# Kernel tuning notes

Hardware: AMD Instinct MI355X
Metric: run time of the kernel (lower is better)

The kernel has to match this reference:

```python
import jax, jax.numpy as jnp
import numpy as np

WS = 11        # gaussian window size
SIGMA = 1.5    # gaussian sigma
L = 10.0       # val_range
SSIM_C1 = (0.01 * L) ** 2
SSIM_C2 = (0.03 * L) ** 2


def _window():
    g = jnp.exp(-((jnp.arange(WS) - WS // 2) ** 2) / (2.0 * SIGMA ** 2))
    g = g / g.sum()
    return jnp.outer(g, g).astype(jnp.float32)  # [11,11], sums to 1


def _blur(z, win):
    # depthwise 11x11 gaussian blur with VALID padding; z: [..., H, W]
    lead = z.shape[:-2]
    zf = z.reshape((-1, 1) + z.shape[-2:])
    out = jax.lax.conv_general_dilated(zf, win[None, None], (1, 1), 'VALID')
    return out.reshape(lead + out.shape[-2:])


def setup_inputs() -> dict:
    key = jax.random.key(0)
    ks = jax.random.split(key, 7)
    B, C, Fc, H, W = 8, 64, 3, 192, 192
    return {
        'x': jax.random.normal(ks[0], (B, C, H, W), jnp.float32),
        'x_feature': jax.random.normal(ks[1], (B, Fc, H, W), jnp.float32),
        'spatial_w': jax.random.normal(ks[2], (1, Fc, 3, 1), jnp.float32) * 0.1,
        'W1': jax.random.normal(ks[3], (C, C), jnp.float32) * 0.05,
        'b1': jnp.zeros((C,), jnp.float32),
        'W2': jax.random.normal(ks[4], (C, C), jnp.float32) * 0.05,
        'b2': jnp.zeros((C,), jnp.float32),
    }


def reference(x, x_feature, spatial_w, W1, b1, W2, b2):
    win = _window()
    # per-channel gaussian moments (computed once, reused across all pairs)
    mu_x = _blur(x, win)                         # [B,C,h,w]
    mu_f = _blur(x_feature, win)                 # [B,F,h,w]
    sig_x = _blur(x * x, win) - mu_x ** 2        # variance of x channels
    sig_f = _blur(x_feature * x_feature, win) - mu_f ** 2
    # all pairwise cross-covariances in one batched blur
    prod = x_feature[:, :, None] * x[:, None]    # [B,F,C,H,W]
    sig_fx = _blur(prod, win) - mu_f[:, :, None] * mu_x[:, None]
    v1 = 2.0 * sig_fx + SSIM_C2
    v2 = sig_f[:, :, None] + sig_x[:, None] + SSIM_C2
    num = (2.0 * mu_f[:, :, None] * mu_x[:, None] + SSIM_C1) * v1
    den = (mu_f[:, :, None] ** 2 + mu_x[:, None] ** 2 + SSIM_C1) * v2
    ssim_info = (num / den).mean(axis=(-2, -1))  # [B,F,C]
    # spatial gate: Conv2d(3,1,(3,1),padding=(1,0)) over [B,F,C,1]
    si4 = ssim_info[..., None]                   # [B,F,C,1]
    h = jax.lax.conv_general_dilated(si4, spatial_w, (1, 1), ((1, 1), (0, 0)))
    h = jax.nn.relu(h).reshape(x.shape[0], -1)   # [B,C]
    h = jax.nn.relu(h @ W1.T + b1) @ W2.T + b2
    return jax.nn.sigmoid(h), ssim_info
```

## Files before the change

### kernel.cpp

```cpp
#include <hip/hip_runtime.h>
#include <math.h>

#define HW 192
#define OW 182
#define NPIX (OW*OW)
#define NTILE 8
#define SSIM_C1 0.01f
#define SSIM_C2 0.09f

#define Gk0 0.0010283835f
#define Gk1 0.0075987615f
#define Gk2 0.0360007700f
#define Gk3 0.1093608000f
#define Gk4 0.2130055400f
#define Gk5 0.2660117000f

typedef float v2f __attribute__((ext_vector_type(2)));

__device__ __forceinline__ v2f vfma(float w, v2f a, v2f b) {
    return __builtin_elementwise_fma((v2f){w, w}, a, b);
}
__device__ __forceinline__ v2f vfma2(v2f w, v2f a, v2f b) {
    return __builtin_elementwise_fma(w, a, b);
}

__device__ __forceinline__ void dgauss(float g[11]) {
    float s = 0.f;
#pragma unroll
    for (int i = 0; i < 11; ++i) {
        float d = (float)(i - 5);
        g[i] = expf(-(d * d) / 4.5f);
        s += g[i];
    }
    float inv = 1.f / s;
#pragma unroll
    for (int i = 0; i < 11; ++i) g[i] *= inv;
}

__global__ __launch_bounds__(256) void muf_kernel(const float* __restrict__ xf,
                                                  float* __restrict__ muf,
                                                  float* __restrict__ sigc2f) {
    const int tile = blockIdx.x % 14;
    const int img  = blockIdx.x / 14;
    const int r0   = tile * 13;

    __shared__ float raw[23][192];
    __shared__ float hb[2][23][184];

    float g[11]; dgauss(g);
    const int t = threadIdx.x;
    const float* src = xf + (size_t)img * HW * HW;

    for (int i = t; i < 23 * 192; i += 256) {
        int rr = i / 192, col = i - rr * 192;
        raw[rr][col] = src[(r0 + rr) * HW + col];
    }
    __syncthreads();

    for (int i = t; i < 23 * OW; i += 256) {
        int rr = i / OW, co = i - rr * OW;
        float a0 = 0.f, a1 = 0.f;
#pragma unroll
        for (int k = 0; k < 11; ++k) {
            float v = raw[rr][co + k];
            float w = g[k];
            a0 += w * v;
            a1 += w * v * v;
        }
        hb[0][rr][co] = a0;
        hb[1][rr][co] = a1;
    }
    __syncthreads();

    for (int i = t; i < 13 * OW; i += 256) {
        int rr = i / OW, co = i - rr * OW;
        float m = 0.f, s2 = 0.f;
#pragma unroll
        for (int k = 0; k < 11; ++k) {
            float w = g[k];
            m  += w * hb[0][rr + k][co];
            s2 += w * hb[1][rr + k][co];
        }
        size_t o = (size_t)img * NPIX + (size_t)(r0 + rr) * OW + co;
        muf[o]    = m;
        sigc2f[o] = s2 - m * m + SSIM_C2;
    }
}

__global__ __launch_bounds__(192, 4) void ssim_kernel(const float* __restrict__ x,
                                                      const float* __restrict__ xf,
                                                      const float* __restrict__ muf,
                                                      const float* __restrict__ sigc2f,
                                                      float* __restrict__ part) {
    const float G[11] = {Gk0,Gk1,Gk2,Gk3,Gk4,Gk5,Gk4,Gk3,Gk2,Gk1,Gk0};
    const v2f WA[6] = {{G[0],0.f},{G[2],G[1]},{G[4],G[3]},{G[6],G[5]},{G[8],G[7]},{G[10],G[9]}};
    const v2f WB[6] = {{G[1],G[0]},{G[3],G[2]},{G[5],G[4]},{G[7],G[6]},{G[9],G[8]},{0.f,G[10]}};

    const int blk  = blockIdx.x;
    const int c    = blk & 63;
    const int tile = (blk >> 6) & 7;
    const int b    = blk >> 9;

    const int out0  = (tile * 182) >> 3;
    const int out1  = ((tile + 1) * 182) >> 3;
    const int n_out = out1 - out0;

    const int t    = threadIdx.x;
    const int half = (t >= 96) ? 1 : 0;
    const int u    = half ? (t - 96) : t;
    const int cu   = 2 * u;
    const bool act = (u <= 90);

    const float* xp  = x  + ((size_t)(b * 64 + c)) * HW * HW + (size_t)out0 * HW + t;
    const float* fp0 = xf + ((size_t)(b * 3 + 0)) * HW * HW + (size_t)out0 * HW + t;
    const float* fp1 = fp0 + HW * HW;
    const float* fp2 = fp1 + HW * HW;

    const float* mp = muf    + (size_t)(b * 3) * NPIX + (size_t)(out0 + half) * OW + cu;
    const float* cp = sigc2f + (size_t)(b * 3) * NPIX + (size_t)(out0 + half) * OW + cu;

    __shared__ float eb[4][5][192];
    __shared__ float red[3][3];

    v2f P01[10], P23[10];
    float P4[10];
#pragma unroll
    for (int j = 0; j < 10; ++j) { P01[j] = (v2f){0.f,0.f}; P23[j] = (v2f){0.f,0.f}; P4[j] = 0.f; }

    v2f A0 = {0.f,0.f}, A1 = {0.f,0.f}, A2 = {0.f,0.f};

    v2f eE01, eE23; float eE4;

    auto vstep = [&](float xv, float a0, float a1, float a2, bool emit) {
        v2f v01 = {xv, xv * xv};
        v2f v23 = {xv * a0, xv * a1};
        float v4 = xv * a2;
        if (emit) {
            eE01 = vfma(G[10], v01, P01[0]);
            eE23 = vfma(G[10], v23, P23[0]);
            eE4  = fmaf(G[10], v4, P4[0]);
        }
#pragma unroll
        for (int j = 0; j < 9; ++j) {
            P01[j] = vfma(G[9 - j], v01, P01[j + 1]);
            P23[j] = vfma(G[9 - j], v23, P23[j + 1]);
            P4[j]  = fmaf(G[9 - j], v4, P4[j + 1]);
        }
        P01[9] = G[0] * v01;
        P23[9] = G[0] * v23;
        P4[9]  = G[0] * v4;
    };

    auto ssim2 = [&](const v2f mux, const v2f sigc,
                     const v2f mf, const v2f cc, const v2f h, v2f& A) {
        const v2f mux2 = mux * mux;
        v2f t1  = mf * mux;
        v2f sfx = h - t1;
        v2f v1s = vfma(2.f, sfx, (v2f){SSIM_C2, SSIM_C2});
        v2f n1  = vfma(2.f, t1, (v2f){SSIM_C1, SSIM_C1});
        v2f num = n1 * v1s;
        v2f qd  = vfma2(mf, mf, (v2f){SSIM_C1, SSIM_C1});
        v2f den = (qd + mux2) * (cc + sigc);
        v2f inv = {__builtin_amdgcn_rcpf(den.x), __builtin_amdgcn_rcpf(den.y)};
        A = vfma2(num, inv, A);
    };

#pragma unroll 1
    for (int r = 0; r < 10; r += 2) {
        float xA = xp[0],  aA0 = fp0[0],  aA1 = fp1[0],  aA2 = fp2[0];
        float xB = xp[HW], aB0 = fp0[HW], aB1 = fp1[HW], aB2 = fp2[HW];
        xp += 2 * HW; fp0 += 2 * HW; fp1 += 2 * HW; fp2 += 2 * HW;
        vstep(xA, aA0, aA1, aA2, false);
        vstep(xB, aB0, aB1, aB2, false);
    }

    const int n_pair = n_out >> 1;

    float xA = xp[0],  aA0 = fp0[0],  aA1 = fp1[0],  aA2 = fp2[0];
    float xB = xp[HW], aB0 = fp0[HW], aB1 = fp1[HW], aB2 = fp2[HW];

#pragma unroll 1
    for (int p = 0; p < n_pair; ++p) {
        const int rb = 2 * (p + 1);
        const int r1 = (rb     < n_out) ? rb     : (n_out - 1);
        const int r2 = (rb + 1 < n_out) ? rb + 1 : (n_out - 1);
        const int o1 = r1 * HW, o2 = r2 * HW;
        const float nxA = xp[o1], naA0 = fp0[o1], naA1 = fp1[o1], naA2 = fp2[o1];
        const float nxB = xp[o2], naB0 = fp0[o2], naB1 = fp1[o2], naB2 = fp2[o2];

        v2f mf0, mf1, mf2, cc0, cc1, cc2;
        if (act) {
            mf0 = *(const v2f*)(mp);
            mf1 = *(const v2f*)(mp + NPIX);
            mf2 = *(const v2f*)(mp + 2 * NPIX);
            cc0 = *(const v2f*)(cp);
            cc1 = *(const v2f*)(cp + NPIX);
            cc2 = *(const v2f*)(cp + 2 * NPIX);
            mp += 2 * OW; cp += 2 * OW;
        }

        const int e = 2 * p;
        const int sA = e & 3, sB = (e + 1) & 3;
        vstep(xA, aA0, aA1, aA2, true);
        eb[sA][0][t] = eE01.x; eb[sA][1][t] = eE01.y;
        eb[sA][2][t] = eE23.x; eb[sA][3][t] = eE23.y;
        eb[sA][4][t] = eE4;
        vstep(xB, aB0, aB1, aB2, true);
        eb[sB][0][t] = eE01.x; eb[sB][1][t] = eE01.y;
        eb[sB][2][t] = eE23.x; eb[sB][3][t] = eE23.y;
        eb[sB][4][t] = eE4;
        __syncthreads();

        xA = nxA; aA0 = naA0; aA1 = naA1; aA2 = naA2;
        xB = nxB; aB0 = naB0; aB1 = naB1; aB2 = naB2;

        if (act) {
            const int sH = half ? sB : sA;
            v2f hacc[5];
#pragma unroll
            for (int f = 0; f < 5; ++f) {
                const float* ep = &eb[sH][f][cu];
                v2f a = {0.f, 0.f};
#pragma unroll
                for (int m = 0; m < 6; ++m) {
                    v2f rd = *(const v2f*)(ep + 2 * m);
                    a = vfma2(WA[m], __builtin_shufflevector(rd, rd, 0, 0), a);
                    a = vfma2(WB[m], __builtin_shufflevector(rd, rd, 1, 1), a);
                }
                hacc[f] = a;
            }
            const v2f mux  = hacc[0];
            const v2f sigc = hacc[1] - mux * mux;
            ssim2(mux, sigc, mf0, cc0, hacc[2], A0);
            ssim2(mux, sigc, mf1, cc1, hacc[3], A1);
            ssim2(mux, sigc, mf2, cc2, hacc[4], A2);
        }
    }

    if (n_out & 1) {
        const int e = n_out - 1;
        vstep(xA, aA0, aA1, aA2, true);
        const int sA = e & 3;
        eb[sA][0][t] = eE01.x; eb[sA][1][t] = eE01.y;
        eb[sA][2][t] = eE23.x; eb[sA][3][t] = eE23.y;
        eb[sA][4][t] = eE4;
        __syncthreads();
        if (act && half == 0) {
            v2f mf0 = *(const v2f*)(mp);
            v2f mf1 = *(const v2f*)(mp + NPIX);
            v2f mf2 = *(const v2f*)(mp + 2 * NPIX);
            v2f cc0 = *(const v2f*)(cp);
            v2f cc1 = *(const v2f*)(cp + NPIX);
            v2f cc2 = *(const v2f*)(cp + 2 * NPIX);
            v2f hacc[5];
#pragma unroll
            for (int f = 0; f < 5; ++f) {
                const float* ep = &eb[sA][f][cu];
                v2f a = {0.f, 0.f};
#pragma unroll
                for (int m = 0; m < 6; ++m) {
                    v2f rd = *(const v2f*)(ep + 2 * m);
                    a = vfma2(WA[m], __builtin_shufflevector(rd, rd, 0, 0), a);
                    a = vfma2(WB[m], __builtin_shufflevector(rd, rd, 1, 1), a);
                }
                hacc[f] = a;
            }
            const v2f mux  = hacc[0];
            const v2f sigc = hacc[1] - mux * mux;
            ssim2(mux, sigc, mf0, cc0, hacc[2], A0);
            ssim2(mux, sigc, mf1, cc1, hacc[3], A1);
            ssim2(mux, sigc, mf2, cc2, hacc[4], A2);
        }
    }

    float acc0 = A0.x + A0.y;
    float acc1 = A1.x + A1.y;
    float acc2 = A2.x + A2.y;
#pragma unroll
    for (int off = 32; off > 0; off >>= 1) {
        acc0 += __shfl_down(acc0, off);
        acc1 += __shfl_down(acc1, off);
        acc2 += __shfl_down(acc2, off);
    }
    const int wid = t >> 6, lane = t & 63;
    if (lane == 0) { red[0][wid] = acc0; red[1][wid] = acc1; red[2][wid] = acc2; }
    __syncthreads();
    if (t == 0) {
        const size_t o = (size_t)tile * 1536 + (size_t)b * 192;
        part[o +   0 + c] = red[0][0] + red[0][1] + red[0][2];
        part[o +  64 + c] = red[1][0] + red[1][1] + red[1][2];
        part[o + 128 + c] = red[2][0] + red[2][1] + red[2][2];
    }
}

__global__ __launch_bounds__(64) void gate_kernel(const float* __restrict__ part,
                                                  const float* __restrict__ sw,
                                                  const float* __restrict__ W1,
                                                  const float* __restrict__ b1,
                                                  const float* __restrict__ W2,
                                                  const float* __restrict__ b2,
                                                  float* __restrict__ out,
                                                  float* __restrict__ out_ssim) {
    const int b = blockIdx.x;
    const int c = threadIdx.x;

    __shared__ float s[3][64];
    __shared__ float h0[64];
    __shared__ float h1[64];

    const float inv = 1.f / (float)NPIX;
#pragma unroll
    for (int f = 0; f < 3; ++f) {
        const int i = b * 192 + f * 64 + c;
        float v = 0.f;
#pragma unroll
        for (int k = 0; k < NTILE; ++k) v += part[i + k * 1536];
        v *= inv;
        s[f][c] = v;
        out_ssim[i] = v;
    }
    __syncthreads();

    float a = 0.f;
#pragma unroll
    for (int f = 0; f < 3; ++f)
#pragma unroll
        for (int i = 0; i < 3; ++i) {
            int cc = c - 1 + i;
            if (cc >= 0 && cc < 64) a += sw[f * 3 + i] * s[f][cc];
        }
    h0[c] = fmaxf(a, 0.f);
    __syncthreads();

    float a1 = b1[c];
    for (int j = 0; j < 64; ++j) a1 += W1[c * 64 + j] * h0[j];
    h1[c] = fmaxf(a1, 0.f);
    __syncthreads();

    float a2 = b2[c];
    for (int j = 0; j < 64; ++j) a2 += W2[c * 64 + j] * h1[j];
    out[b * 64 + c] = 1.f / (1.f + expf(-a2));
}

extern "C" void kernel_launch(void* const* d_in, const int* in_sizes, int n_in,
                              void* d_out, int out_size, void* d_ws, size_t ws_size,
                              hipStream_t stream) {
    const float* x  = (const float*)d_in[0];
    const float* xf = (const float*)d_in[1];
    const float* sw = (const float*)d_in[2];
    const float* W1 = (const float*)d_in[3];
    const float* b1 = (const float*)d_in[4];
    const float* W2 = (const float*)d_in[5];
    const float* b2 = (const float*)d_in[6];
    float* out = (float*)d_out;

    float* muf  = (float*)d_ws;
    float* sigf = muf + 24 * NPIX;
    float* part = sigf + 24 * NPIX;

    muf_kernel <<<24 * 14,        256, 0, stream>>>(xf, muf, sigf);
    ssim_kernel<<<8 * 64 * NTILE, 192, 0, stream>>>(x, xf, muf, sigf, part);
    gate_kernel<<<8,               64, 0, stream>>>(part, sw, W1, b1, W2, b2, out, out + 512);
}
```

Before: 108.5 us.

## Software-pipeline vertical blur with horizontal pass across shared-memory slots

Restructures the main loop so the vertical blur and shared-memory store for the next row pair overlap with the horizontal blur and SSIM math on the current pair. A prologue fills slots 0/1 first, and each iteration needs one barrier instead of a barrier between producing and consuming. Part of the LDS reads are issued before the vstep work to hide their latency. This raises register pressure (30 v2f LDS values held in flight) and adds more intricate slot and row-index bookkeeping.

```diff
diff --git a/kernel.cpp b/kernel.cpp
--- a/kernel.cpp
+++ b/kernel.cpp
@@ -104,6 +104,7 @@
     const int out0  = (tile * 182) >> 3;
     const int out1  = ((tile + 1) * 182) >> 3;
     const int n_out = out1 - out0;
+    const int n_in  = n_out + 10;
 
     const int t    = threadIdx.x;
     const int half = (t >= 96) ? 1 : 0;
@@ -151,9 +152,18 @@
         P4[9]  = G[0] * v4;
     };
 
-    auto ssim2 = [&](const v2f mux, const v2f sigc,
+    auto hblur = [&](const v2f rd[6]) {
+        v2f a = {0.f, 0.f};
+#pragma unroll
+        for (int m = 0; m < 6; ++m) {
+            a = vfma2(WA[m], __builtin_shufflevector(rd[m], rd[m], 0, 0), a);
+            a = vfma2(WB[m], __builtin_shufflevector(rd[m], rd[m], 1, 1), a);
+        }
+        return a;
+    };
+
+    auto ssim2 = [&](const v2f mux, const v2f mux2, const v2f sigc,
                      const v2f mf, const v2f cc, const v2f h, v2f& A) {
-        const v2f mux2 = mux * mux;
         v2f t1  = mf * mux;
         v2f sfx = h - t1;
         v2f v1s = vfma(2.f, sfx, (v2f){SSIM_C2, SSIM_C2});
@@ -165,6 +175,12 @@
         A = vfma2(num, inv, A);
     };
 
+    auto store_e = [&](int slot) {
+        eb[slot][0][t] = eE01.x; eb[slot][1][t] = eE01.y;
+        eb[slot][2][t] = eE23.x; eb[slot][3][t] = eE23.y;
+        eb[slot][4][t] = eE4;
+    };
+
 #pragma unroll 1
     for (int r = 0; r < 10; r += 2) {
         float xA = xp[0],  aA0 = fp0[0],  aA1 = fp1[0],  aA2 = fp2[0];
@@ -176,17 +192,26 @@
 
     const int n_pair = n_out >> 1;
 
-    float xA = xp[0],  aA0 = fp0[0],  aA1 = fp1[0],  aA2 = fp2[0];
-    float xB = xp[HW], aB0 = fp0[HW], aB1 = fp1[HW], aB2 = fp2[HW];
+    {
+        float xA = xp[0],  aA0 = fp0[0],  aA1 = fp1[0],  aA2 = fp2[0];
+        float xB = xp[HW], aB0 = fp0[HW], aB1 = fp1[HW], aB2 = fp2[HW];
+        xp += 2 * HW; fp0 += 2 * HW; fp1 += 2 * HW; fp2 += 2 * HW;
+        vstep(xA, aA0, aA1, aA2, true);  store_e(0);
+        vstep(xB, aB0, aB1, aB2, true);  store_e(1);
+    }
+    float cxA = xp[0],  cA0 = fp0[0],  cA1 = fp1[0],  cA2 = fp2[0];
+    float cxB = xp[HW], cB0 = fp0[HW], cB1 = fp1[HW], cB2 = fp2[HW];
+    xp += 2 * HW; fp0 += 2 * HW; fp1 += 2 * HW; fp2 += 2 * HW;
+    __syncthreads();
 
 #pragma unroll 1
     for (int p = 0; p < n_pair; ++p) {
-        const int rb = 2 * (p + 1);
-        const int r1 = (rb     < n_out) ? rb     : (n_out - 1);
-        const int r2 = (rb + 1 < n_out) ? rb + 1 : (n_out - 1);
-        const int o1 = r1 * HW, o2 = r2 * HW;
-        const float nxA = xp[o1], naA0 = fp0[o1], naA1 = fp1[o1], naA2 = fp2[o1];
-        const float nxB = xp[o2], naB0 = fp0[o2], naB1 = fp1[o2], naB2 = fp2[o2];
+        const int ri = 14 + 2 * p;
+        const int o1 = ((ri     < n_in) ? 0 : (n_in - 1 - ri))     * HW;
+        const int o2 = ((ri + 1 < n_in) ? 1 : (n_in - 1 - ri))     * HW;
+        const float nxA = xp[o1], nA0 = fp0[o1], nA1 = fp1[o1], nA2 = fp2[o1];
+        const float nxB = xp[o2], nB0 = fp0[o2], nB1 = fp1[o2], nB2 = fp2[o2];
+        xp += 2 * HW; fp0 += 2 * HW; fp1 += 2 * HW; fp2 += 2 * HW;
 
         v2f mf0, mf1, mf2, cc0, cc1, cc2;
         if (act) {
@@ -199,52 +224,45 @@
             mp += 2 * OW; cp += 2 * OW;
         }
 
-        const int e = 2 * p;
-        const int sA = e & 3, sB = (e + 1) & 3;
-        vstep(xA, aA0, aA1, aA2, true);
-        eb[sA][0][t] = eE01.x; eb[sA][1][t] = eE01.y;
-        eb[sA][2][t] = eE23.x; eb[sA][3][t] = eE23.y;
-        eb[sA][4][t] = eE4;
-        vstep(xB, aB0, aB1, aB2, true);
-        eb[sB][0][t] = eE01.x; eb[sB][1][t] = eE01.y;
-        eb[sB][2][t] = eE23.x; eb[sB][3][t] = eE23.y;
-        eb[sB][4][t] = eE4;
+        const int sA = (2 * p) & 3, sB = sA | 1;
+        const int sH = half ? sB : sA;
+
+        v2f rd0[6], rd1[6], rd2[6];
+#pragma unroll
+        for (int m = 0; m < 6; ++m) rd0[m] = *(const v2f*)(&eb[sH][0][cu] + 2 * m);
+#pragma unroll
+        for (int m = 0; m < 6; ++m) rd1[m] = *(const v2f*)(&eb[sH][1][cu] + 2 * m);
+#pragma unroll
+        for (int m = 0; m < 6; ++m) rd2[m] = *(const v2f*)(&eb[sH][2][cu] + 2 * m);
+
+        const bool dov = (p + 1 < n_pair) || (n_out & 1);
+        if (dov) {
+            const int wA = (2 * p + 2) & 3, wB = wA | 1;
+            vstep(cxA, cA0, cA1, cA2, true);  store_e(wA);
+            vstep(cxB, cB0, cB1, cB2, true);  store_e(wB);
+        }
+        cxA = nxA; cA0 = nA0; cA1 = nA1; cA2 = nA2;
+        cxB = nxB; cB0 = nB0; cB1 = nB1; cB2 = nB2;
+
+        v2f rd3[6], rd4[6];
+#pragma unroll
+        for (int m = 0; m < 6; ++m) rd3[m] = *(const v2f*)(&eb[sH][3][cu] + 2 * m);
+#pragma unroll
+        for (int m = 0; m < 6; ++m) rd4[m] = *(const v2f*)(&eb[sH][4][cu] + 2 * m);
+
+        if (act) {
+            const v2f mux  = hblur(rd0);
+            const v2f mux2 = mux * mux;
+            const v2f sigc = hblur(rd1) - mux2;
+            ssim2(mux, mux2, sigc, mf0, cc0, hblur(rd2), A0);
+            ssim2(mux, mux2, sigc, mf1, cc1, hblur(rd3), A1);
+            ssim2(mux, mux2, sigc, mf2, cc2, hblur(rd4), A2);
+        }
         __syncthreads();
-
-        xA = nxA; aA0 = naA0; aA1 = naA1; aA2 = naA2;
-        xB = nxB; aB0 = naB0; aB1 = naB1; aB2 = naB2;
-
-        if (act) {
-            const int sH = half ? sB : sA;
-            v2f hacc[5];
-#pragma unroll
-            for (int f = 0; f < 5; ++f) {
-                const float* ep = &eb[sH][f][cu];
-                v2f a = {0.f, 0.f};
-#pragma unroll
-                for (int m = 0; m < 6; ++m) {
-                    v2f rd = *(const v2f*)(ep + 2 * m);
-                    a = vfma2(WA[m], __builtin_shufflevector(rd, rd, 0, 0), a);
-                    a = vfma2(WB[m], __builtin_shufflevector(rd, rd, 1, 1), a);
-                }
-                hacc[f] = a;
-            }
-            const v2f mux  = hacc[0];
-            const v2f sigc = hacc[1] - mux * mux;
-            ssim2(mux, sigc, mf0, cc0, hacc[2], A0);
-            ssim2(mux, sigc, mf1, cc1, hacc[3], A1);
-            ssim2(mux, sigc, mf2, cc2, hacc[4], A2);
-        }
     }
 
     if (n_out & 1) {
-        const int e = n_out - 1;
-        vstep(xA, aA0, aA1, aA2, true);
-        const int sA = e & 3;
-        eb[sA][0][t] = eE01.x; eb[sA][1][t] = eE01.y;
-        eb[sA][2][t] = eE23.x; eb[sA][3][t] = eE23.y;
-        eb[sA][4][t] = eE4;
-        __syncthreads();
+        const int sA = (n_out - 1) & 3;
         if (act && half == 0) {
             v2f mf0 = *(const v2f*)(mp);
             v2f mf1 = *(const v2f*)(mp + NPIX);
@@ -252,25 +270,23 @@
             v2f cc0 = *(const v2f*)(cp);
             v2f cc1 = *(const v2f*)(cp + NPIX);
             v2f cc2 = *(const v2f*)(cp + 2 * NPIX);
-            v2f hacc[5];
-#pragma unroll
-            for (int f = 0; f < 5; ++f) {
-                const float* ep = &eb[sA][f][cu];
-                v2f a = {0.f, 0.f};
-#pragma unroll
-                for (int m = 0; m < 6; ++m) {
-                    v2f rd = *(const v2f*)(ep + 2 * m);
-                    a = vfma2(WA[m], __builtin_shufflevector(rd, rd, 0, 0), a);
-                    a = vfma2(WB[m], __builtin_shufflevector(rd, rd, 1, 1), a);
-                }
-                hacc[f] = a;
+            v2f rd0[6], rd1[6], rd2[6], rd3[6], rd4[6];
+#pragma unroll
+            for (int m = 0; m < 6; ++m) {
+                rd0[m] = *(const v2f*)(&eb[sA][0][cu] + 2 * m);
+                rd1[m] = *(const v2f*)(&eb[sA][1][cu] + 2 * m);
+                rd2[m] = *(const v2f*)(&eb[sA][2][cu] + 2 * m);
+                rd3[m] = *(const v2f*)(&eb[sA][3][cu] + 2 * m);
+                rd4[m] = *(const v2f*)(&eb[sA][4][cu] + 2 * m);
             }
-            const v2f mux  = hacc[0];
-            const v2f sigc = hacc[1] - mux * mux;
-            ssim2(mux, sigc, mf0, cc0, hacc[2], A0);
-            ssim2(mux, sigc, mf1, cc1, hacc[3], A1);
-            ssim2(mux, sigc, mf2, cc2, hacc[4], A2);
-        }
+            const v2f mux  = hblur(rd0);
+            const v2f mux2 = mux * mux;
+            const v2f sigc = hblur(rd1) - mux2;
+            ssim2(mux, mux2, sigc, mf0, cc0, hblur(rd2), A0);
+            ssim2(mux, mux2, sigc, mf1, cc1, hblur(rd3), A1);
+            ssim2(mux, mux2, sigc, mf2, cc2, hblur(rd4), A2);
+        }
+        __syncthreads();
     }
 
     float acc0 = A0.x + A0.y;
```

Measured after the change: 207.9 us. 1.92x slower.
